# Kernel optimization log

Measured on AMD Instinct MI355X. Metric: run time of the kernel, lower is better.

## Reference

```python
import jax, jax.numpy as jnp
import numpy as np

B = 32768
SEQ_LEN = 24
H = 64            # HIDDEN_DIM
SLOTS = 8         # MEMORY_SLOTS
VOCAB = 64        # VOCAB_SIZE


def setup_inputs() -> dict:
    key = jax.random.key(0)
    ks = jax.random.split(key, 8)
    seqs = jax.random.randint(ks[0], (B, SEQ_LEN), 0, VOCAB, dtype=jnp.int64)
    query_tok = jax.random.randint(ks[1], (B,), 0, VOCAB + 2, dtype=jnp.int64)
    embed = jax.random.normal(ks[2], (VOCAB + 2, H), dtype=jnp.float32) * 0.05
    gw1 = jax.random.normal(ks[3], (2 * H, 32), dtype=jnp.float32) / np.sqrt(2 * H)
    gb1 = jnp.zeros((32,), jnp.float32)
    gw2 = jax.random.normal(ks[4], (32, 1), dtype=jnp.float32) / np.sqrt(32)
    gb2 = jnp.zeros((1,), jnp.float32)
    rw1 = jax.random.normal(ks[5], (2 * H, H), dtype=jnp.float32) / np.sqrt(2 * H)
    rb1 = jnp.zeros((H,), jnp.float32)
    rw2 = jax.random.normal(ks[6], (H, VOCAB), dtype=jnp.float32) / np.sqrt(H)
    rb2 = jnp.zeros((VOCAB,), jnp.float32)
    return {"seqs": seqs, "query_tok": query_tok, "embed": embed,
            "gw1": gw1, "gb1": gb1, "gw2": gw2, "gb2": gb2,
            "rw1": rw1, "rb1": rb1, "rw2": rw2, "rb2": rb2}


def reference(seqs, query_tok, embed, gw1, gb1, gw2, gb2, rw1, rb1, rw2, rb2):
    Bb = seqs.shape[0]
    T = SEQ_LEN - 1  # model writes tokens 0..SEQ_LEN-2 into memory
    embs = embed[seqs[:, :T]]                     # [B, T, H]
    batch_idx = jnp.arange(Bb)

    def step(mem, xs):
        t, emb = xs                               # emb: [B, H]
        ctx = jnp.broadcast_to(emb[:, None, :], mem.shape)
        pair = jnp.concatenate([ctx, mem], axis=-1)        # [B, S, 2H]
        h = jax.nn.relu(pair @ gw1 + gb1)                  # [B, S, 32]
        score = jax.nn.sigmoid(h @ gw2 + gb2)[..., 0]      # [B, S]
        # while memory not full, fill slot t; otherwise evict argmax score
        idx = jnp.where(t < SLOTS, t, jnp.argmax(score, axis=1))
        mem = mem.at[batch_idx, idx].set(emb)
        return mem, None

    mem0 = jnp.zeros((Bb, SLOTS, H), embed.dtype)
    mem, _ = jax.lax.scan(step, mem0, (jnp.arange(T), jnp.swapaxes(embs, 0, 1)))

    summary = mem.mean(axis=1)                    # [B, H]  (memory is full: T > SLOTS)
    q = embed[query_tok]                          # [B, H]
    x = jnp.concatenate([q, summary], axis=-1)    # [B, 2H]
    logits = jax.nn.relu(x @ rw1 + rb1) @ rw2 + rb2   # [B, VOCAB]
    return logits
```

## Files before the change

kernel.cpp:

```cpp
#include <hip/hip_runtime.h>
#include <math.h>

typedef __attribute__((ext_vector_type(8))) _Float16 f16x8;
typedef __attribute__((ext_vector_type(4))) float f32x4;

#define TSTEPS 23
#define ROWS 128

#define WSB_B1 0
#define WSB_W2 21504
#define WSB_Z  30720

__global__ __launch_bounds__(256) void pre_all(
    const float* __restrict__ embed, const float* __restrict__ gw1,
    const float* __restrict__ gb1, const float* __restrict__ gw2,
    const float* __restrict__ gb2, const float* __restrict__ rw1,
    const float* __restrict__ rb1, const float* __restrict__ rw2,
    char* __restrict__ wsc)
{
    __shared__ float sEmb[66 * 64];
    __shared__ float sW[128 * 64];
    __shared__ float sV[64 * 33];
    __shared__ float sU[4 * 32];
    __shared__ float sG[65];
    __shared__ float sRb1[64];

    const int tid = threadIdx.x;
    const int blk = blockIdx.x;

    if (blk < 16) {
        {
            const float4* es = (const float4*)embed;
            float4* ed = (float4*)sEmb;
            for (int i = tid; i < 1024; i += 256) ed[i] = es[i];
            const float4* gs = (const float4*)gw1;
            float4* gd = (float4*)sW;
            for (int i = tid; i < 1024; i += 256) gd[i] = gs[i];
            if (tid < 32) { sG[tid] = gb1[tid]; sG[32 + tid] = gw2[tid]; }
            if (tid == 64) sG[64] = gb2[0];
        }
        __syncthreads();
        {
            const int s = tid >> 2, j0 = (tid & 3) * 8;
            float4 er[16];
            const float4* erp = (const float4*)(sEmb + s * 64);
            #pragma unroll
            for (int q = 0; q < 16; ++q) er[q] = erp[q];
            float acc[8] = {0.f, 0.f, 0.f, 0.f, 0.f, 0.f, 0.f, 0.f};
            #pragma unroll
            for (int k = 0; k < 64; ++k) {
                const float ek = ((const float*)er)[k];
                const float4 w0 = *(const float4*)&sW[(64 + k) * 32 + j0];
                const float4 w1 = *(const float4*)&sW[(64 + k) * 32 + j0 + 4];
                acc[0] = fmaf(ek, w0.x, acc[0]); acc[1] = fmaf(ek, w0.y, acc[1]);
                acc[2] = fmaf(ek, w0.z, acc[2]); acc[3] = fmaf(ek, w0.w, acc[3]);
                acc[4] = fmaf(ek, w1.x, acc[4]); acc[5] = fmaf(ek, w1.y, acc[5]);
                acc[6] = fmaf(ek, w1.z, acc[6]); acc[7] = fmaf(ek, w1.w, acc[7]);
            }
            #pragma unroll
            for (int jj = 0; jj < 8; ++jj) sV[s * 33 + jj + j0] = acc[jj];
        }
        if (tid < 128) {
            const int cc = tid >> 5, j = tid & 31;
            const int c = blk * 4 + cc;
            float acc = 0.f;
            const float* er = sEmb + c * 64;
            #pragma unroll
            for (int k = 0; k < 64; ++k)
                acc = fmaf(er[k], sW[k * 32 + j], acc);
            sU[cc * 32 + j] = acc;
        }
        __syncthreads();
        {
            const int cc = tid >> 6, s = tid & 63;
            const int c = blk * 4 + cc;
            float ur[32], vr[32];
            #pragma unroll
            for (int j = 0; j < 32; ++j) { ur[j] = sU[cc * 32 + j]; vr[j] = sV[s * 33 + j]; }
            double p0 = 0.0, p1 = 0.0, p2 = 0.0, p3 = 0.0;
            #pragma unroll
            for (int j = 0; j < 32; j += 4) {
                const double a0 = (double)ur[j]     + (double)vr[j]     + (double)sG[j];
                const double a1 = (double)ur[j + 1] + (double)vr[j + 1] + (double)sG[j + 1];
                const double a2 = (double)ur[j + 2] + (double)vr[j + 2] + (double)sG[j + 2];
                const double a3 = (double)ur[j + 3] + (double)vr[j + 3] + (double)sG[j + 3];
                if (a0 > 0.0) p0 += a0 * (double)sG[32 + j];
                if (a1 > 0.0) p1 += a1 * (double)sG[32 + j + 1];
                if (a2 > 0.0) p2 += a2 * (double)sG[32 + j + 2];
                if (a3 > 0.0) p3 += a3 * (double)sG[32 + j + 3];
            }
            const double z = (double)sG[64] + ((p0 + p1) + (p2 + p3));
            ((float*)(wsc + WSB_Z))[c * 64 + s] = (float)z;
        }
    } else if (blk < 49) {
        {
            const float4* es = (const float4*)embed;
            float4* ed = (float4*)sEmb;
            for (int i = tid; i < 1056; i += 256) ed[i] = es[i];
            const float4* rs = (const float4*)rw1;
            float4* rd = (float4*)sW;
            for (int i = tid; i < 2048; i += 256) rd[i] = rs[i];
            if (tid < 64) sRb1[tid] = rb1[tid];
        }
        __syncthreads();
        const int e = (blk - 16) * 256 + tid;
        if (e < 8320) {
            const int n = e & 63, k = e >> 6;
            const int trow = (k < 64) ? k : (k - 64);
            const int ofs = (k < 64) ? 64 : 0;
            float4 er[16];
            const float4* erp = (const float4*)(sEmb + trow * 64);
            #pragma unroll
            for (int q = 0; q < 16; ++q) er[q] = erp[q];
            float acc = (k < 64) ? 0.f : sRb1[n];
            #pragma unroll
            for (int m = 0; m < 64; ++m)
                acc = fmaf(((const float*)er)[m], sW[(ofs + m) * 64 + n], acc);
            acc *= (k < 64) ? (0.125f * 256.f) : 256.f;
            ((_Float16*)(wsc + WSB_B1))[n * 168 + k] = (_Float16)acc;
        }
    } else {
        _Float16* w2t = (_Float16*)(wsc + WSB_W2);
        for (int e = tid; e < 4096; e += 256) {
            const int n = e & 63, j = e >> 6;
            w2t[n * 72 + j] = (_Float16)rw2[j * 64 + n];
        }
        _Float16* b1 = (_Float16*)(wsc + WSB_B1);
        for (int e = tid; e < 2432; e += 256) {
            const int n = e / 38, k = 130 + (e - n * 38);
            b1[n * 168 + k] = (_Float16)0.f;
        }
    }
}

__device__ __forceinline__ f16x8 build_slot_win(const unsigned* s, const unsigned* hb, int ko)
{
    unsigned w0 = 0, w1 = 0, w2 = 0, w3 = 0;
    #pragma unroll
    for (int i = 0; i < 8; ++i) {
        const unsigned d = s[i] - (unsigned)ko;
        const unsigned val = (d < 8u) ? (hb[i] << ((d & 1u) * 16)) : 0u;
        const unsigned q = d >> 1;
        w0 |= (q == 0u) ? val : 0u;
        w1 |= (q == 1u) ? val : 0u;
        w2 |= (q == 2u) ? val : 0u;
        w3 |= (q == 3u) ? val : 0u;
    }
    union { unsigned u[4]; f16x8 v; } r;
    r.u[0] = w0; r.u[1] = w1; r.u[2] = w2; r.u[3] = w3;
    return r.v;
}

__device__ __forceinline__ f16x8 build_q_win(int kq, int ko)
{
    const unsigned d = (unsigned)(kq - ko);
    const unsigned val = (d < 8u) ? (0x3C00u << ((d & 1u) * 16)) : 0u;
    const unsigned q = d >> 1;
    union { unsigned u[4]; f16x8 v; } r;
    r.u[0] = (q == 0u) ? val : 0u;
    r.u[1] = (q == 1u) ? val : 0u;
    r.u[2] = (q == 2u) ? val : 0u;
    r.u[3] = (q == 3u) ? val : 0u;
    return r.v;
}

#define L_Z    0
#define L_B1   16640
#define L_W2   38144
#define L_H    47360
#define L_ROW  65792
#define L_RB2  67840

__global__ __launch_bounds__(512) void sm_main(
    const int* __restrict__ seqs, const int* __restrict__ qtok,
    const float* __restrict__ rb2, const char* __restrict__ wsc,
    float* __restrict__ out)
{
    __shared__ __align__(16) char smem[68096];
    float*    sZ   = (float*)(smem + L_Z);
    _Float16* sB1  = (_Float16*)(smem + L_B1);
    _Float16* sW2  = (_Float16*)(smem + L_W2);
    _Float16* sH   = (_Float16*)(smem + L_H);
    uint4*    sRow = (uint4*)(smem + L_ROW);
    float*    sRb2 = (float*)(smem + L_RB2);

    const int tid = threadIdx.x;
    const int base = blockIdx.x * ROWS;

    unsigned pk[6];
    int qt = 0;
    if (tid < ROWS) {
        const int4* sq = (const int4*)(seqs + (size_t)(base + tid) * 24);
        #pragma unroll
        for (int i = 0; i < 6; ++i) {
            const int4 w4 = sq[i];
            pk[i] = (unsigned)w4.x | ((unsigned)w4.y << 8) |
                    ((unsigned)w4.z << 16) | ((unsigned)w4.w << 24);
        }
        qt = qtok[base + tid];
    }

    {
        const float* zsrc = (const float*)(wsc + WSB_Z);
        #pragma unroll
        for (int i = 0; i < 8; ++i) {
            const int e = tid + i * 512;
            sZ[(e >> 6) * 65 + (e & 63)] = zsrc[e];
        }
        if (tid < 64) sRb2[tid] = rb2[tid];
    }
    __syncthreads();

    if (tid < ROWS) {
        unsigned lo = pk[0], hi = pk[1];
        #pragma unroll
        for (int t = 8; t < TSTEPS; ++t) {
            const int c = (int)((pk[t >> 2] >> ((t & 3) * 8)) & 255u);
            const float* zr = sZ + c * 65;
            float b = zr[lo & 63]; int am = 0; float z;
            z = zr[(lo >> 8) & 63];  if (z > b) { b = z; am = 1; }
            z = zr[(lo >> 16) & 63]; if (z > b) { b = z; am = 2; }
            z = zr[lo >> 24];        if (z > b) { b = z; am = 3; }
            z = zr[hi & 63];         if (z > b) { b = z; am = 4; }
            z = zr[(hi >> 8) & 63];  if (z > b) { b = z; am = 5; }
            z = zr[(hi >> 16) & 63]; if (z > b) { b = z; am = 6; }
            z = zr[hi >> 24];        if (z > b) { b = z; am = 7; }
            const unsigned cb = (unsigned)c;
            if (am < 4) { const int sh = am * 8; lo = (lo & ~(255u << sh)) | (cb << sh); }
            else        { const int sh = am * 8 - 32; hi = (hi & ~(255u << sh)) | (cb << sh); }
        }
        int t_[8] = { (int)(lo & 63), (int)((lo >> 8) & 63), (int)((lo >> 16) & 63), (int)(lo >> 24),
                      (int)(hi & 63), (int)((hi >> 8) & 63), (int)((hi >> 16) & 63), (int)(hi >> 24) };
        int tot[8] = {1, 1, 1, 1, 1, 1, 1, 1};
        #pragma unroll
        for (int i = 0; i < 8; ++i)
            #pragma unroll
            for (int j = i + 1; j < 8; ++j) {
                const int eq = (t_[i] == t_[j]);
                tot[i] += eq; tot[j] += eq;
            }
        unsigned tp = 0;
        #pragma unroll
        for (int i = 0; i < 8; ++i) tp |= (unsigned)tot[i] << (4 * i);
        sRow[tid] = make_uint4(lo & 0x3F3F3F3Fu, hi & 0x3F3F3F3Fu, tp, (unsigned)qt);
    } else {
        const int t2 = tid - 128;
        const float4* b1s = (const float4*)(wsc + WSB_B1);
        float4* b1d = (float4*)sB1;
        for (int i = t2; i < 1344; i += 384) b1d[i] = b1s[i];
        const float4* w2s = (const float4*)(wsc + WSB_W2);
        float4* w2d = (float4*)sW2;
        for (int i = t2; i < 576; i += 384) w2d[i] = w2s[i];
    }
    __syncthreads();

    const int lane = tid & 63;
    const int w = tid >> 6;
    const int c16 = lane & 15, g = lane >> 4;
    const int arow = w * 16 + c16;

    unsigned sl[8], hb[8];
    int kq;
    {
        const uint4 ri = sRow[arow];
        sl[0] = ri.x & 63u; sl[1] = (ri.x >> 8) & 63u;
        sl[2] = (ri.x >> 16) & 63u; sl[3] = ri.x >> 24;
        sl[4] = ri.y & 63u; sl[5] = (ri.y >> 8) & 63u;
        sl[6] = (ri.y >> 16) & 63u; sl[7] = ri.y >> 24;
        #pragma unroll
        for (int i = 0; i < 8; ++i) {
            const unsigned tot = (ri.z >> (4 * i)) & 15u;
            union { _Float16 h; unsigned short b; } cv;
            cv.h = (_Float16)(float)tot;
            hb[i] = (unsigned)cv.b;
        }
        kq = 64 + (int)ri.w;
    }

    f32x4 a0 = {0.f, 0.f, 0.f, 0.f}, a1 = a0, a2 = a0, a3 = a0;
    #pragma unroll
    for (int ks = 0; ks < 5; ++ks) {
        const int ko = ks * 32 + g * 8;
        const f16x8 af = (ks < 2) ? build_slot_win(sl, hb, ko) : build_q_win(kq, ko);
        const f16x8 b0 = *(const f16x8*)&sB1[(c16) * 168 + ko];
        const f16x8 b1 = *(const f16x8*)&sB1[(16 + c16) * 168 + ko];
        const f16x8 b2 = *(const f16x8*)&sB1[(32 + c16) * 168 + ko];
        const f16x8 b3 = *(const f16x8*)&sB1[(48 + c16) * 168 + ko];
        a0 = __builtin_amdgcn_mfma_f32_16x16x32_f16(af, b0, a0, 0, 0, 0);
        a1 = __builtin_amdgcn_mfma_f32_16x16x32_f16(af, b1, a1, 0, 0, 0);
        a2 = __builtin_amdgcn_mfma_f32_16x16x32_f16(af, b2, a2, 0, 0, 0);
        a3 = __builtin_amdgcn_mfma_f32_16x16x32_f16(af, b3, a3, 0, 0, 0);
    }
    {
        const int rbase = w * 16 + g * 4;
        #pragma unroll
        for (int j = 0; j < 4; ++j) {
            _Float16* hr = sH + (rbase + j) * 72;
            const float v0 = a0[j], v1 = a1[j], v2 = a2[j], v3 = a3[j];
            hr[c16]      = (_Float16)(v0 > 0.f ? v0 : 0.f);
            hr[16 + c16] = (_Float16)(v1 > 0.f ? v1 : 0.f);
            hr[32 + c16] = (_Float16)(v2 > 0.f ? v2 : 0.f);
            hr[48 + c16] = (_Float16)(v3 > 0.f ? v3 : 0.f);
        }
    }
    __syncthreads();

    f32x4 d0 = {0.f, 0.f, 0.f, 0.f}, d1 = d0, d2 = d0, d3 = d0;
    #pragma unroll
    for (int ks = 0; ks < 2; ++ks) {
        const int ko = ks * 32 + g * 8;
        const f16x8 af = *(const f16x8*)&sH[arow * 72 + ko];
        const f16x8 b0 = *(const f16x8*)&sW2[(c16) * 72 + ko];
        const f16x8 b1 = *(const f16x8*)&sW2[(16 + c16) * 72 + ko];
        const f16x8 b2 = *(const f16x8*)&sW2[(32 + c16) * 72 + ko];
        const f16x8 b3 = *(const f16x8*)&sW2[(48 + c16) * 72 + ko];
        d0 = __builtin_amdgcn_mfma_f32_16x16x32_f16(af, b0, d0, 0, 0, 0);
        d1 = __builtin_amdgcn_mfma_f32_16x16x32_f16(af, b1, d1, 0, 0, 0);
        d2 = __builtin_amdgcn_mfma_f32_16x16x32_f16(af, b2, d2, 0, 0, 0);
        d3 = __builtin_amdgcn_mfma_f32_16x16x32_f16(af, b3, d3, 0, 0, 0);
    }
    float* sOut = (float*)(void*)smem;
    {
        const int rbase = w * 16 + g * 4;
        #pragma unroll
        for (int j = 0; j < 4; ++j) {
            float* orow = sOut + (rbase + j) * 68;
            orow[c16]      = d0[j] * (1.f / 256.f) + sRb2[c16];
            orow[16 + c16] = d1[j] * (1.f / 256.f) + sRb2[16 + c16];
            orow[32 + c16] = d2[j] * (1.f / 256.f) + sRb2[32 + c16];
            orow[48 + c16] = d3[j] * (1.f / 256.f) + sRb2[48 + c16];
        }
    }
    __syncthreads();

    #pragma unroll
    for (int r2 = 0; r2 < 4; ++r2) {
        const int idx = r2 * 512 + tid;
        const int row = idx >> 4, c4 = idx & 15;
        *(float4*)(out + (size_t)(base + row) * 64 + c4 * 4) =
            *(const float4*)&sOut[row * 68 + c4 * 4];
    }
}

extern "C" void kernel_launch(void* const* d_in, const int* in_sizes, int n_in,
                              void* d_out, int out_size, void* d_ws, size_t ws_size,
                              hipStream_t stream)
{
    const int* seqs    = (const int*)d_in[0];
    const int* qtok    = (const int*)d_in[1];
    const float* embed = (const float*)d_in[2];
    const float* gw1   = (const float*)d_in[3];
    const float* gb1   = (const float*)d_in[4];
    const float* gw2   = (const float*)d_in[5];
    const float* gb2   = (const float*)d_in[6];
    const float* rw1   = (const float*)d_in[7];
    const float* rb1   = (const float*)d_in[8];
    const float* rw2   = (const float*)d_in[9];
    const float* rb2   = (const float*)d_in[10];
    char* wsc  = (char*)d_ws;
    float* out = (float*)d_out;
    const int B = in_sizes[1];

    pre_all<<<50, 256, 0, stream>>>(embed, gw1, gb1, gw2, gb2, rw1, rb1, rw2, wsc);
    sm_main<<<B / ROWS, 512, 0, stream>>>(seqs, qtok, rb2, wsc, out);
}
```

Before: 19.69 us.

## Process 256 rows per block and store logits directly from registers

```diff
diff --git a/kernel.cpp b/kernel.cpp
--- a/kernel.cpp
+++ b/kernel.cpp
@@ -5,7 +5,7 @@
 typedef __attribute__((ext_vector_type(4))) float f32x4;
 
 #define TSTEPS 23
-#define ROWS 128
+#define ROWS 256
 
 #define WSB_B1 0
 #define WSB_W2 21504
@@ -168,15 +168,15 @@
 #define L_B1   16640
 #define L_W2   38144
 #define L_H    47360
-#define L_ROW  65792
-#define L_RB2  67840
+#define L_ROW  84224
+#define L_RB2  88320
 
 __global__ __launch_bounds__(512) void sm_main(
     const int* __restrict__ seqs, const int* __restrict__ qtok,
     const float* __restrict__ rb2, const char* __restrict__ wsc,
     float* __restrict__ out)
 {
-    __shared__ __align__(16) char smem[68096];
+    __shared__ __align__(16) char smem[88576];
     float*    sZ   = (float*)(smem + L_Z);
     _Float16* sB1  = (_Float16*)(smem + L_B1);
     _Float16* sW2  = (_Float16*)(smem + L_W2);
@@ -244,55 +244,55 @@
         for (int i = 0; i < 8; ++i) tp |= (unsigned)tot[i] << (4 * i);
         sRow[tid] = make_uint4(lo & 0x3F3F3F3Fu, hi & 0x3F3F3F3Fu, tp, (unsigned)qt);
     } else {
-        const int t2 = tid - 128;
+        const int t2 = tid - 256;
         const float4* b1s = (const float4*)(wsc + WSB_B1);
         float4* b1d = (float4*)sB1;
-        for (int i = t2; i < 1344; i += 384) b1d[i] = b1s[i];
+        for (int i = t2; i < 1344; i += 256) b1d[i] = b1s[i];
         const float4* w2s = (const float4*)(wsc + WSB_W2);
         float4* w2d = (float4*)sW2;
-        for (int i = t2; i < 576; i += 384) w2d[i] = w2s[i];
+        for (int i = t2; i < 576; i += 256) w2d[i] = w2s[i];
     }
     __syncthreads();
 
     const int lane = tid & 63;
     const int w = tid >> 6;
     const int c16 = lane & 15, g = lane >> 4;
-    const int arow = w * 16 + c16;
-
-    unsigned sl[8], hb[8];
-    int kq;
-    {
-        const uint4 ri = sRow[arow];
-        sl[0] = ri.x & 63u; sl[1] = (ri.x >> 8) & 63u;
-        sl[2] = (ri.x >> 16) & 63u; sl[3] = ri.x >> 24;
-        sl[4] = ri.y & 63u; sl[5] = (ri.y >> 8) & 63u;
-        sl[6] = (ri.y >> 16) & 63u; sl[7] = ri.y >> 24;
-        #pragma unroll
-        for (int i = 0; i < 8; ++i) {
-            const unsigned tot = (ri.z >> (4 * i)) & 15u;
-            union { _Float16 h; unsigned short b; } cv;
-            cv.h = (_Float16)(float)tot;
-            hb[i] = (unsigned)cv.b;
-        }
-        kq = 64 + (int)ri.w;
-    }
-
-    f32x4 a0 = {0.f, 0.f, 0.f, 0.f}, a1 = a0, a2 = a0, a3 = a0;
+
     #pragma unroll
-    for (int ks = 0; ks < 5; ++ks) {
-        const int ko = ks * 32 + g * 8;
-        const f16x8 af = (ks < 2) ? build_slot_win(sl, hb, ko) : build_q_win(kq, ko);
-        const f16x8 b0 = *(const f16x8*)&sB1[(c16) * 168 + ko];
-        const f16x8 b1 = *(const f16x8*)&sB1[(16 + c16) * 168 + ko];
-        const f16x8 b2 = *(const f16x8*)&sB1[(32 + c16) * 168 + ko];
-        const f16x8 b3 = *(const f16x8*)&sB1[(48 + c16) * 168 + ko];
-        a0 = __builtin_amdgcn_mfma_f32_16x16x32_f16(af, b0, a0, 0, 0, 0);
-        a1 = __builtin_amdgcn_mfma_f32_16x16x32_f16(af, b1, a1, 0, 0, 0);
-        a2 = __builtin_amdgcn_mfma_f32_16x16x32_f16(af, b2, a2, 0, 0, 0);
-        a3 = __builtin_amdgcn_mfma_f32_16x16x32_f16(af, b3, a3, 0, 0, 0);
-    }
-    {
-        const int rbase = w * 16 + g * 4;
+    for (int rt = 0; rt < 2; ++rt) {
+        const int arow = rt * 128 + w * 16 + c16;
+        unsigned sl[8], hb[8];
+        int kq;
+        {
+            const uint4 ri = sRow[arow];
+            sl[0] = ri.x & 63u; sl[1] = (ri.x >> 8) & 63u;
+            sl[2] = (ri.x >> 16) & 63u; sl[3] = ri.x >> 24;
+            sl[4] = ri.y & 63u; sl[5] = (ri.y >> 8) & 63u;
+            sl[6] = (ri.y >> 16) & 63u; sl[7] = ri.y >> 24;
+            #pragma unroll
+            for (int i = 0; i < 8; ++i) {
+                const unsigned tot = (ri.z >> (4 * i)) & 15u;
+                union { _Float16 h; unsigned short b; } cv;
+                cv.h = (_Float16)(float)tot;
+                hb[i] = (unsigned)cv.b;
+            }
+            kq = 64 + (int)ri.w;
+        }
+        f32x4 a0 = {0.f, 0.f, 0.f, 0.f}, a1 = a0, a2 = a0, a3 = a0;
+        #pragma unroll
+        for (int ks = 0; ks < 5; ++ks) {
+            const int ko = ks * 32 + g * 8;
+            const f16x8 af = (ks < 2) ? build_slot_win(sl, hb, ko) : build_q_win(kq, ko);
+            const f16x8 b0 = *(const f16x8*)&sB1[(c16) * 168 + ko];
+            const f16x8 b1 = *(const f16x8*)&sB1[(16 + c16) * 168 + ko];
+            const f16x8 b2 = *(const f16x8*)&sB1[(32 + c16) * 168 + ko];
+            const f16x8 b3 = *(const f16x8*)&sB1[(48 + c16) * 168 + ko];
+            a0 = __builtin_amdgcn_mfma_f32_16x16x32_f16(af, b0, a0, 0, 0, 0);
+            a1 = __builtin_amdgcn_mfma_f32_16x16x32_f16(af, b1, a1, 0, 0, 0);
+            a2 = __builtin_amdgcn_mfma_f32_16x16x32_f16(af, b2, a2, 0, 0, 0);
+            a3 = __builtin_amdgcn_mfma_f32_16x16x32_f16(af, b3, a3, 0, 0, 0);
+        }
+        const int rbase = rt * 128 + w * 16 + g * 4;
         #pragma unroll
         for (int j = 0; j < 4; ++j) {
             _Float16* hr = sH + (rbase + j) * 72;
@@ -305,40 +305,33 @@
     }
     __syncthreads();
 
-    f32x4 d0 = {0.f, 0.f, 0.f, 0.f}, d1 = d0, d2 = d0, d3 = d0;
+    const float r0 = sRb2[c16], r1 = sRb2[16 + c16], r2_ = sRb2[32 + c16], r3 = sRb2[48 + c16];
     #pragma unroll
-    for (int ks = 0; ks < 2; ++ks) {
-        const int ko = ks * 32 + g * 8;
-        const f16x8 af = *(const f16x8*)&sH[arow * 72 + ko];
-        const f16x8 b0 = *(const f16x8*)&sW2[(c16) * 72 + ko];
-        const f16x8 b1 = *(const f16x8*)&sW2[(16 + c16) * 72 + ko];
-        const f16x8 b2 = *(const f16x8*)&sW2[(32 + c16) * 72 + ko];
-        const f16x8 b3 = *(const f16x8*)&sW2[(48 + c16) * 72 + ko];
-        d0 = __builtin_amdgcn_mfma_f32_16x16x32_f16(af, b0, d0, 0, 0, 0);
-        d1 = __builtin_amdgcn_mfma_f32_16x16x32_f16(af, b1, d1, 0, 0, 0);
-        d2 = __builtin_amdgcn_mfma_f32_16x16x32_f16(af, b2, d2, 0, 0, 0);
-        d3 = __builtin_amdgcn_mfma_f32_16x16x32_f16(af, b3, d3, 0, 0, 0);
-    }
-    float* sOut = (float*)(void*)smem;
-    {
-        const int rbase = w * 16 + g * 4;
+    for (int rt = 0; rt < 2; ++rt) {
+        const int arow = rt * 128 + w * 16 + c16;
+        f32x4 d0 = {0.f, 0.f, 0.f, 0.f}, d1 = d0, d2 = d0, d3 = d0;
+        #pragma unroll
+        for (int ks = 0; ks < 2; ++ks) {
+            const int ko = ks * 32 + g * 8;
+            const f16x8 af = *(const f16x8*)&sH[arow * 72 + ko];
+            const f16x8 b0 = *(const f16x8*)&sW2[(c16) * 72 + ko];
+            const f16x8 b1 = *(const f16x8*)&sW2[(16 + c16) * 72 + ko];
+            const f16x8 b2 = *(const f16x8*)&sW2[(32 + c16) * 72 + ko];
+            const f16x8 b3 = *(const f16x8*)&sW2[(48 + c16) * 72 + ko];
+            d0 = __builtin_amdgcn_mfma_f32_16x16x32_f16(af, b0, d0, 0, 0, 0);
+            d1 = __builtin_amdgcn_mfma_f32_16x16x32_f16(af, b1, d1, 0, 0, 0);
+            d2 = __builtin_amdgcn_mfma_f32_16x16x32_f16(af, b2, d2, 0, 0, 0);
+            d3 = __builtin_amdgcn_mfma_f32_16x16x32_f16(af, b3, d3, 0, 0, 0);
+        }
+        const int rbase = rt * 128 + w * 16 + g * 4;
         #pragma unroll
         for (int j = 0; j < 4; ++j) {
-            float* orow = sOut + (rbase + j) * 68;
-            orow[c16]      = d0[j] * (1.f / 256.f) + sRb2[c16];
-            orow[16 + c16] = d1[j] * (1.f / 256.f) + sRb2[16 + c16];
-            orow[32 + c16] = d2[j] * (1.f / 256.f) + sRb2[32 + c16];
-            orow[48 + c16] = d3[j] * (1.f / 256.f) + sRb2[48 + c16];
-        }
-    }
-    __syncthreads();
-
-    #pragma unroll
-    for (int r2 = 0; r2 < 4; ++r2) {
-        const int idx = r2 * 512 + tid;
-        const int row = idx >> 4, c4 = idx & 15;
-        *(float4*)(out + (size_t)(base + row) * 64 + c4 * 4) =
-            *(const float4*)&sOut[row * 68 + c4 * 4];
+            float* orow = out + (size_t)(base + rbase + j) * 64;
+            orow[c16]      = d0[j] * (1.f / 256.f) + r0;
+            orow[16 + c16] = d1[j] * (1.f / 256.f) + r1;
+            orow[32 + c16] = d2[j] * (1.f / 256.f) + r2_;
+            orow[48 + c16] = d3[j] * (1.f / 256.f) + r3;
+        }
     }
 }
 
```

Measured after the change: 21.61 us. +9.7%, slower.
